# Optimization experiments

Measured on AMD Instinct MI355X. Metric: run time of the kernel, lower is better.

The kernel has to match this reference:

```python
import jax, jax.numpy as jnp
import numpy as np

W_IMPORTANCE = 0.1  # from __init__ default
EPS = 1e-12         # F.normalize eps


def _l2norm(x):
    n = jnp.sqrt(jnp.sum(x * x, axis=1, keepdims=True))
    return x / jnp.maximum(n, EPS)


def setup_inputs() -> dict:
    key = jax.random.key(0)
    k1, k2, k3 = jax.random.split(key, 3)
    return {
        "target_edge_feats": jax.random.normal(k1, (16384, 512), dtype=jnp.float32),
        "source_edge_feats": jax.random.normal(k2, (32768, 512), dtype=jnp.float32),
        "source_importance": jax.random.uniform(k3, (32768,), dtype=jnp.float32),
        "topk": 8,
        "chunk_size": 4096,
    }


def reference(target_edge_feats, source_edge_feats, source_importance, topk, chunk_size):
    E_t, Fdim = target_edge_feats.shape
    tn = _l2norm(target_edge_feats)            # [E_t, F]
    sn = _l2norm(source_edge_feats)            # [E_s, F]
    bias = W_IMPORTANCE * source_importance    # [E_s]

    n_chunks = E_t // chunk_size               # E_t chosen as exact multiple
    t_chunks = tn.reshape(n_chunks, chunk_size, Fdim)

    def per_chunk(t):
        # cosine similarity + importance bias, then top-k over sources
        score = jnp.einsum('cf,ef->ce', t, sn) + bias[None, :]  # [chunk, E_s]
        vals, idx = jax.lax.top_k(score, topk)
        return vals, idx

    vals, idx = jax.lax.map(per_chunk, t_chunks)  # [n_chunks, chunk, K]
    topk_score = vals.reshape(E_t, topk)
    topk_idx = idx.reshape(E_t, topk)
    topk_alpha = jax.nn.softmax(topk_score, axis=-1)
    return (topk_idx, topk_score, topk_alpha)
```

## Files before the change

### kernel.cpp

```cpp
#include <hip/hip_runtime.h>
#include <hip/hip_bf16.h>
#include <float.h>

#define KDIM 512
#define MBLK 64
#define NBLK 256
#define KBLK 16
#define NTH  256
#define APAD 68
#define BROW 284
#define TOPK 8
#define BIDX(c) ((c) + (((c) >> 5) << 2))

__device__ __forceinline__ float bf16_rne_f32(float v) {
  return __bfloat162float(__float2bfloat16(v));
}

__global__ void er_norms(const float* __restrict__ T, const float* __restrict__ S,
                         float* __restrict__ nt, float* __restrict__ ns,
                         int M, int N) {
  int gid = blockIdx.x * blockDim.x + threadIdx.x;
  int row = gid >> 2;
  int b   = gid & 3;
  if (row >= M + N) return;
  const float* base = (row < M) ? (T + (size_t)row * KDIM)
                                : (S + (size_t)(row - M) * KDIM);
  const float4* p4 = (const float4*)(base + b * 128);
  float r[8];
  {
    float4 f0 = p4[0], f1 = p4[1];
    r[0] = __fmul_rn(f0.x, f0.x); r[1] = __fmul_rn(f0.y, f0.y);
    r[2] = __fmul_rn(f0.z, f0.z); r[3] = __fmul_rn(f0.w, f0.w);
    r[4] = __fmul_rn(f1.x, f1.x); r[5] = __fmul_rn(f1.y, f1.y);
    r[6] = __fmul_rn(f1.z, f1.z); r[7] = __fmul_rn(f1.w, f1.w);
  }
  #pragma unroll
  for (int i = 2; i < 32; i += 2) {
    float4 f0 = p4[i], f1 = p4[i + 1];
    r[0] = __fadd_rn(r[0], __fmul_rn(f0.x, f0.x));
    r[1] = __fadd_rn(r[1], __fmul_rn(f0.y, f0.y));
    r[2] = __fadd_rn(r[2], __fmul_rn(f0.z, f0.z));
    r[3] = __fadd_rn(r[3], __fmul_rn(f0.w, f0.w));
    r[4] = __fadd_rn(r[4], __fmul_rn(f1.x, f1.x));
    r[5] = __fadd_rn(r[5], __fmul_rn(f1.y, f1.y));
    r[6] = __fadd_rn(r[6], __fmul_rn(f1.z, f1.z));
    r[7] = __fadd_rn(r[7], __fmul_rn(f1.w, f1.w));
  }
  float B = __fadd_rn(__fadd_rn(__fadd_rn(r[0], r[1]), __fadd_rn(r[2], r[3])),
                      __fadd_rn(__fadd_rn(r[4], r[5]), __fadd_rn(r[6], r[7])));
  float t = __fadd_rn(B, __shfl_xor(B, 1, 64));
  float s = __fadd_rn(t, __shfl_xor(t, 2, 64));
  if (b == 0) {
    float nr = __fsqrt_rn(s);
    if (row < M) nt[row] = nr; else ns[row - M] = nr;
  }
}

__global__ void er_prep(const float* __restrict__ X, const float* __restrict__ nrm,
                        float* __restrict__ XT, int R) {
  __shared__ float t[64][68];
  const int r0 = blockIdx.x * 64, c0 = blockIdx.y * 64;
  const int tx = threadIdx.x & 15, ty = threadIdx.x >> 4;
  #pragma unroll
  for (int q = 0; q < 4; ++q) {
    int r = r0 + ty + q * 16;
    float dn = fmaxf(nrm[r], 1e-12f);
    float4 v = *(const float4*)&X[(size_t)r * KDIM + c0 + tx * 4];
    t[ty + q*16][tx*4+0] = __fdiv_rn(v.x, dn);
    t[ty + q*16][tx*4+1] = __fdiv_rn(v.y, dn);
    t[ty + q*16][tx*4+2] = __fdiv_rn(v.z, dn);
    t[ty + q*16][tx*4+3] = __fdiv_rn(v.w, dn);
  }
  __syncthreads();
  #pragma unroll
  for (int q = 0; q < 4; ++q) {
    int c = c0 + ty + q * 16;
    float4 o;
    o.x = t[tx*4+0][ty + q*16];
    o.y = t[tx*4+1][ty + q*16];
    o.z = t[tx*4+2][ty + q*16];
    o.w = t[tx*4+3][ty + q*16];
    *(float4*)&XT[(size_t)c * R + r0 + tx * 4] = o;
  }
}

__global__ __launch_bounds__(NTH, 2)
void er_cand_fast(const float* __restrict__ ATN, const float* __restrict__ SNT,
                  const float* __restrict__ imp,
                  float* __restrict__ pval, int* __restrict__ pidx,
                  int M, int N, int nsplit, int mblocks) {
  __shared__ float b_lds[KBLK][NBLK];
  __shared__ float tval[MBLK][TOPK];
  __shared__ int   tidx[MBLK][TOPK];
  __shared__ float tthr[MBLK];

  const int tid    = threadIdx.x;
  const int mb     = blockIdx.x % mblocks;
  const int split  = blockIdx.x / mblocks;
  const int m_base = mb * MBLK;
  const int n_cols = N / nsplit;
  const int n_start = split * n_cols;
  const int ntiles  = n_cols / NBLK;
  const int lane = tid & 63;
  const int w = __builtin_amdgcn_readfirstlane(tid >> 6);

  if (tid < MBLK) {
    tthr[tid] = -FLT_MAX;
    #pragma unroll
    for (int j = 0; j < TOPK; ++j) { tval[tid][j] = -FLT_MAX; tidx[tid][j] = 0; }
  }
  __syncthreads();

  const float* aw = ATN + m_base + w * 16;

  #pragma unroll 1
  for (int t = 0; t < ntiles; ++t) {
    const int n_base = n_start + t * NBLK;
    float acc[16][4];
    #pragma unroll
    for (int i = 0; i < 16; ++i)
      #pragma unroll
      for (int j = 0; j < 4; ++j) acc[i][j] = 0.f;

    float4 br[4];
    #pragma unroll
    for (int ii = 0; ii < 4; ++ii)
      br[ii] = *(const float4*)&SNT[(size_t)(w + 4*ii) * N + n_base + lane * 4];

    #pragma unroll 1
    for (int kc = 0; kc < KDIM / KBLK; ++kc) {
      __syncthreads();
      #pragma unroll
      for (int ii = 0; ii < 4; ++ii)
        *(float4*)&b_lds[w + 4*ii][lane * 4] = br[ii];
      __syncthreads();
      if (kc + 1 < KDIM / KBLK) {
        #pragma unroll
        for (int ii = 0; ii < 4; ++ii)
          br[ii] = *(const float4*)&SNT[(size_t)((kc+1)*KBLK + w + 4*ii) * N
                                        + n_base + lane * 4];
      }
      #pragma unroll
      for (int k = 0; k < KBLK; ++k) {
        const float4* ap = (const float4*)(aw + (size_t)(kc * KBLK + k) * M);
        float4 a0 = ap[0], a1 = ap[1], a2 = ap[2], a3 = ap[3];
        float4 b  = *(const float4*)&b_lds[k][lane * 4];
        float av[16] = {a0.x,a0.y,a0.z,a0.w, a1.x,a1.y,a1.z,a1.w,
                        a2.x,a2.y,a2.z,a2.w, a3.x,a3.y,a3.z,a3.w};
        float bw4[4] = {b.x, b.y, b.z, b.w};
        #pragma unroll
        for (int i = 0; i < 16; ++i)
          #pragma unroll
          for (int j = 0; j < 4; ++j)
            acc[i][j] = fmaf(av[i], bw4[j], acc[i][j]);
      }
    }

    float4 impv = *(const float4*)&imp[n_base + lane * 4];
    float bv[4] = {__fmul_rn(0.1f, impv.x), __fmul_rn(0.1f, impv.y),
                   __fmul_rn(0.1f, impv.z), __fmul_rn(0.1f, impv.w)};
    int need = 0;
    #pragma unroll
    for (int i = 0; i < 16; ++i) {
      float thr = tthr[w * 16 + i];
      #pragma unroll
      for (int j = 0; j < 4; ++j) {
        float s = __fadd_rn(acc[i][j], bv[j]);
        need |= (s > thr) ? 1 : 0;
      }
    }
    unsigned long long mask = __ballot(need);
    while (mask) {
      int cur = __ffsll(mask) - 1;
      mask &= mask - 1;
      if (lane == cur) {
        #pragma unroll
        for (int i = 0; i < 16; ++i) {
          int r = w * 16 + i;
          #pragma unroll
          for (int j = 0; j < 4; ++j) {
            float s = __fadd_rn(acc[i][j], bv[j]);
            if (s > tthr[r]) {
              int p = TOPK - 1;
              while (p > 0 && tval[r][p-1] < s) {
                tval[r][p] = tval[r][p-1];
                tidx[r][p] = tidx[r][p-1];
                --p;
              }
              tval[r][p] = s;
              tidx[r][p] = n_base + lane * 4 + j;
              tthr[r] = tval[r][TOPK-1];
            }
          }
        }
      }
    }
  }

  __syncthreads();
  for (int r = tid; r < MBLK; r += NTH) {
    size_t off = ((size_t)split * M + m_base + r) * TOPK;
    #pragma unroll
    for (int j = 0; j < TOPK; ++j) { pval[off + j] = tval[r][j]; pidx[off + j] = tidx[r][j]; }
  }
}

__global__ __launch_bounds__(NTH, 2)
void er_cand_div(const float* __restrict__ A, const float* __restrict__ B,
                 const float* __restrict__ imp,
                 const float* __restrict__ nt, const float* __restrict__ ns,
                 float* __restrict__ pval, int* __restrict__ pidx,
                 int M, int N, int nsplit, int mblocks) {
  __shared__ float a_lds[KBLK][APAD];
  __shared__ float b_lds[KBLK][BROW];
  __shared__ float tval[MBLK][TOPK];
  __shared__ int   tidx[MBLK][TOPK];
  __shared__ float tthr[MBLK];

  const int tid    = threadIdx.x;
  const int mb     = blockIdx.x % mblocks;
  const int split  = blockIdx.x / mblocks;
  const int m_base = mb * MBLK;
  const int n_cols = N / nsplit;
  const int n_start = split * n_cols;
  const int ntiles  = n_cols / NBLK;
  const int tm = tid >> 5;
  const int tn = tid & 31;
  const int lane = tid & 63;

  if (tid < MBLK) {
    tthr[tid] = -FLT_MAX;
    #pragma unroll
    for (int j = 0; j < TOPK; ++j) { tval[tid][j] = -FLT_MAX; tidx[tid][j] = 0; }
  }
  __syncthreads();

  const int sarow = tid >> 2, saks = tid & 3;
  const int bread_off = BIDX(tn * 8);

  #pragma unroll 1
  for (int t = 0; t < ntiles; ++t) {
    const int n_base = n_start + t * NBLK;
    float acc[8][8];
    #pragma unroll
    for (int i = 0; i < 8; ++i)
      #pragma unroll
      for (int j = 0; j < 8; ++j) acc[i][j] = 0.f;

    float4 ar, br[4];
    ar = *(const float4*)&A[(size_t)(m_base + sarow) * KDIM + saks * 4];
    #pragma unroll
    for (int ii = 0; ii < 4; ++ii) {
      int u = tid + NTH * ii, row = u >> 2, ks = u & 3;
      br[ii] = *(const float4*)&B[(size_t)(n_base + row) * KDIM + ks * 4];
    }

    #pragma unroll 1
    for (int kc = 0; kc < KDIM / KBLK; ++kc) {
      __syncthreads();
      {
        float dn = fmaxf(nt[m_base + sarow], 1e-12f);
        a_lds[saks*4+0][sarow] = __fdiv_rn(ar.x, dn);
        a_lds[saks*4+1][sarow] = __fdiv_rn(ar.y, dn);
        a_lds[saks*4+2][sarow] = __fdiv_rn(ar.z, dn);
        a_lds[saks*4+3][sarow] = __fdiv_rn(ar.w, dn);
      }
      #pragma unroll
      for (int ii = 0; ii < 4; ++ii) {
        int u = tid + NTH * ii, row = u >> 2, ks = u & 3;
        float dn = fmaxf(ns[n_base + row], 1e-12f);
        int c = BIDX(row);
        b_lds[ks*4+0][c] = __fdiv_rn(br[ii].x, dn);
        b_lds[ks*4+1][c] = __fdiv_rn(br[ii].y, dn);
        b_lds[ks*4+2][c] = __fdiv_rn(br[ii].z, dn);
        b_lds[ks*4+3][c] = __fdiv_rn(br[ii].w, dn);
      }
      __syncthreads();
      if (kc + 1 < KDIM / KBLK) {
        int kb = (kc + 1) * KBLK;
        ar = *(const float4*)&A[(size_t)(m_base + sarow) * KDIM + kb + saks * 4];
        #pragma unroll
        for (int ii = 0; ii < 4; ++ii) {
          int u = tid + NTH * ii, row = u >> 2, ks = u & 3;
          br[ii] = *(const float4*)&B[(size_t)(n_base + row) * KDIM + kb + ks * 4];
        }
      }
      #pragma unroll 16
      for (int k = 0; k < KBLK; ++k) {
        const float4* ap = (const float4*)&a_lds[k][tm * 8];
        const float4* bp = (const float4*)&b_lds[k][bread_off];
        float4 a0 = ap[0], a1 = ap[1], b0 = bp[0], b1 = bp[1];
        float av[8] = {a0.x,a0.y,a0.z,a0.w,a1.x,a1.y,a1.z,a1.w};
        float bw[8] = {b0.x,b0.y,b0.z,b0.w,b1.x,b1.y,b1.z,b1.w};
        #pragma unroll
        for (int i = 0; i < 8; ++i)
          #pragma unroll
          for (int j = 0; j < 8; ++j)
            acc[i][j] = fmaf(av[i], bw[j], acc[i][j]);
      }
    }

    float bv[8];
    #pragma unroll
    for (int j = 0; j < 8; ++j) bv[j] = __fmul_rn(0.1f, imp[n_base + tn * 8 + j]);

    int need = 0;
    #pragma unroll
    for (int i = 0; i < 8; ++i) {
      float thr = tthr[tm * 8 + i];
      #pragma unroll
      for (int j = 0; j < 8; ++j) {
        float s = __fadd_rn(acc[i][j], bv[j]);
        need |= (s > thr) ? 1 : 0;
      }
    }
    unsigned long long mask = __ballot(need);
    while (mask) {
      int cur = __ffsll(mask) - 1;
      mask &= mask - 1;
      if (lane == cur) {
        #pragma unroll
        for (int i = 0; i < 8; ++i) {
          int r = tm * 8 + i;
          #pragma unroll
          for (int j = 0; j < 8; ++j) {
            float s = __fadd_rn(acc[i][j], bv[j]);
            if (s > tthr[r]) {
              int p = TOPK - 1;
              while (p > 0 && tval[r][p-1] < s) {
                tval[r][p] = tval[r][p-1];
                tidx[r][p] = tidx[r][p-1];
                --p;
              }
              tval[r][p] = s;
              tidx[r][p] = n_base + tn * 8 + j;
              tthr[r] = tval[r][TOPK-1];
            }
          }
        }
      }
    }
  }

  __syncthreads();
  for (int r = tid; r < MBLK; r += NTH) {
    size_t off = ((size_t)split * M + m_base + r) * TOPK;
    #pragma unroll
    for (int j = 0; j < TOPK; ++j) { pval[off + j] = tval[r][j]; pidx[off + j] = tidx[r][j]; }
  }
}

__global__ void er_merge(const float* __restrict__ pval, const int* __restrict__ pidx,
                         float* __restrict__ out, int M, int nsplit) {
  int m = blockIdx.x * blockDim.x + threadIdx.x;
  if (m >= M) return;
  int heads[4] = {0, 0, 0, 0};
  float v[TOPK]; int id[TOPK];
  for (int o = 0; o < TOPK; ++o) {
    float bvv = -FLT_MAX; int bi = 0x7fffffff; int bs = 0;
    for (int s = 0; s < nsplit; ++s) {
      if (heads[s] < TOPK) {
        size_t off = ((size_t)s * M + m) * TOPK + heads[s];
        float vv = pval[off]; int ii = pidx[off];
        if (vv > bvv || (vv == bvv && ii < bi)) { bvv = vv; bi = ii; bs = s; }
      }
    }
    v[o] = bvv; id[o] = bi; heads[bs]++;
  }
  float mx = v[0];
  float e[TOPK];
  #pragma unroll
  for (int j = 0; j < TOPK; ++j) e[j] = expf(__fadd_rn(v[j], -mx));
  float sum = __fadd_rn(
      __fadd_rn(__fadd_rn(e[0], e[1]), __fadd_rn(e[2], e[3])),
      __fadd_rn(__fadd_rn(e[4], e[5]), __fadd_rn(e[6], e[7])));
  const size_t SEC  = (size_t)M * TOPK;
  const size_t base = (size_t)m * TOPK;
  #pragma unroll
  for (int j = 0; j < TOPK; ++j) {
    out[base + j]         = bf16_rne_f32((float)id[j]);
    out[SEC + base + j]   = bf16_rne_f32(v[j]);
    out[2*SEC + base + j] = bf16_rne_f32(__fdiv_rn(e[j], sum));
  }
}

extern "C" void kernel_launch(void* const* d_in, const int* in_sizes, int n_in,
                              void* d_out, int out_size, void* d_ws, size_t ws_size,
                              hipStream_t stream) {
  const float* T   = (const float*)d_in[0];
  const float* S   = (const float*)d_in[1];
  const float* imp = (const float*)d_in[2];
  int M = in_sizes[0] / KDIM;
  int N = in_sizes[1] / KDIM;
  int mblocks = M / MBLK;

  char* ws = (char*)d_ws;
  float* nt = (float*)ws;
  float* ns = nt + M;
  size_t off_pval = (size_t)(M + N) * 4;
  size_t off_pidx = off_pval + (size_t)4 * M * TOPK * 4;
  size_t off_atn  = off_pidx + (size_t)4 * M * TOPK * 4;
  size_t off_snt  = off_atn + (size_t)M * KDIM * 4;
  size_t full_need = off_snt + (size_t)N * KDIM * 4;

  float* pval = (float*)(ws + off_pval);
  int*   pidx = (int*)(ws + off_pidx);
  float* out  = (float*)d_out;

  er_norms<<<(4 * (M + N) + 255) / 256, 256, 0, stream>>>(T, S, nt, ns, M, N);

  if (ws_size >= full_need) {
    float* ATN = (float*)(ws + off_atn);
    float* SNT = (float*)(ws + off_snt);
    er_prep<<<dim3(M / 64, KDIM / 64), 256, 0, stream>>>(T, nt, ATN, M);
    er_prep<<<dim3(N / 64, KDIM / 64), 256, 0, stream>>>(S, ns, SNT, N);
    er_cand_fast<<<mblocks * 4, NTH, 0, stream>>>(ATN, SNT, imp,
                                                  pval, pidx, M, N, 4, mblocks);
    er_merge<<<(M + 255) / 256, 256, 0, stream>>>(pval, pidx, out, M, 4);
  } else {
    int nsplit = 4;
    while (nsplit > 1) {
      size_t need = (size_t)(M + N) * 4 + (size_t)nsplit * M * TOPK * 8;
      if (need <= ws_size) break;
      nsplit >>= 1;
    }
    er_cand_div<<<mblocks * nsplit, NTH, 0, stream>>>(T, S, imp, nt, ns,
                                                      pval, pidx, M, N, nsplit, mblocks);
    er_merge<<<(M + 255) / 256, 256, 0, stream>>>(pval, pidx, out, M, nsplit);
  }
}
```

Measured before the change: 11.01 ms.

## Stage A tile in LDS and use 8x8 register blocking in candidate GEMM

The candidate-scoring kernel now stages the A (target) tile in shared memory alongside B, instead of each wave reading A directly from global memory every k step. Each thread computes an 8x8 register tile (8 rows by two groups of 4 columns) rather than 16x4, which improves arithmetic intensity per LDS load. The top-k insertion also gains index-based tie-breaking (lower index wins on equal scores) and uses >= in the filter, which may trigger the serial insertion path slightly more often.

```diff
diff --git a/kernel.cpp b/kernel.cpp
--- a/kernel.cpp
+++ b/kernel.cpp
@@ -85,10 +85,11 @@
 }
 
 __global__ __launch_bounds__(NTH, 2)
-void er_cand_fast(const float* __restrict__ ATN, const float* __restrict__ SNT,
-                  const float* __restrict__ imp,
-                  float* __restrict__ pval, int* __restrict__ pidx,
-                  int M, int N, int nsplit, int mblocks) {
+void er_cand_fast2(const float* __restrict__ ATN, const float* __restrict__ SNT,
+                   const float* __restrict__ imp,
+                   float* __restrict__ pval, int* __restrict__ pidx,
+                   int M, int N, int nsplit, int mblocks) {
+  __shared__ float a_lds[KBLK][APAD];
   __shared__ float b_lds[KBLK][NBLK];
   __shared__ float tval[MBLK][TOPK];
   __shared__ int   tidx[MBLK][TOPK];
@@ -101,72 +102,85 @@
   const int n_cols = N / nsplit;
   const int n_start = split * n_cols;
   const int ntiles  = n_cols / NBLK;
+  const int tm = tid >> 5;
+  const int tn = tid & 31;
   const int lane = tid & 63;
-  const int w = __builtin_amdgcn_readfirstlane(tid >> 6);
 
   if (tid < MBLK) {
     tthr[tid] = -FLT_MAX;
     #pragma unroll
-    for (int j = 0; j < TOPK; ++j) { tval[tid][j] = -FLT_MAX; tidx[tid][j] = 0; }
+    for (int j = 0; j < TOPK; ++j) { tval[tid][j] = -FLT_MAX; tidx[tid][j] = 0x7fffffff; }
   }
   __syncthreads();
 
-  const float* aw = ATN + m_base + w * 16;
+  const int arow = tid >> 4, acol = (tid & 15) * 4;
 
   #pragma unroll 1
   for (int t = 0; t < ntiles; ++t) {
     const int n_base = n_start + t * NBLK;
-    float acc[16][4];
-    #pragma unroll
-    for (int i = 0; i < 16; ++i)
-      #pragma unroll
-      for (int j = 0; j < 4; ++j) acc[i][j] = 0.f;
-
-    float4 br[4];
-    #pragma unroll
-    for (int ii = 0; ii < 4; ++ii)
-      br[ii] = *(const float4*)&SNT[(size_t)(w + 4*ii) * N + n_base + lane * 4];
+    float acc[8][8];
+    #pragma unroll
+    for (int i = 0; i < 8; ++i)
+      #pragma unroll
+      for (int j = 0; j < 8; ++j) acc[i][j] = 0.f;
+
+    float4 ar, br[4];
+    ar = *(const float4*)&ATN[(size_t)arow * M + m_base + acol];
+    #pragma unroll
+    for (int ii = 0; ii < 4; ++ii) {
+      int u = tid + NTH * ii, brow = u >> 6, bcol = (u & 63) * 4;
+      br[ii] = *(const float4*)&SNT[(size_t)brow * N + n_base + bcol];
+    }
 
     #pragma unroll 1
     for (int kc = 0; kc < KDIM / KBLK; ++kc) {
       __syncthreads();
-      #pragma unroll
-      for (int ii = 0; ii < 4; ++ii)
-        *(float4*)&b_lds[w + 4*ii][lane * 4] = br[ii];
+      *(float4*)&a_lds[arow][acol] = ar;
+      #pragma unroll
+      for (int ii = 0; ii < 4; ++ii) {
+        int u = tid + NTH * ii, brow = u >> 6, bcol = (u & 63) * 4;
+        *(float4*)&b_lds[brow][bcol] = br[ii];
+      }
       __syncthreads();
       if (kc + 1 < KDIM / KBLK) {
-        #pragma unroll
-        for (int ii = 0; ii < 4; ++ii)
-          br[ii] = *(const float4*)&SNT[(size_t)((kc+1)*KBLK + w + 4*ii) * N
-                                        + n_base + lane * 4];
+        int kb = (kc + 1) * KBLK;
+        ar = *(const float4*)&ATN[(size_t)(kb + arow) * M + m_base + acol];
+        #pragma unroll
+        for (int ii = 0; ii < 4; ++ii) {
+          int u = tid + NTH * ii, brow = u >> 6, bcol = (u & 63) * 4;
+          br[ii] = *(const float4*)&SNT[(size_t)(kb + brow) * N + n_base + bcol];
+        }
       }
       #pragma unroll
       for (int k = 0; k < KBLK; ++k) {
-        const float4* ap = (const float4*)(aw + (size_t)(kc * KBLK + k) * M);
-        float4 a0 = ap[0], a1 = ap[1], a2 = ap[2], a3 = ap[3];
-        float4 b  = *(const float4*)&b_lds[k][lane * 4];
-        float av[16] = {a0.x,a0.y,a0.z,a0.w, a1.x,a1.y,a1.z,a1.w,
-                        a2.x,a2.y,a2.z,a2.w, a3.x,a3.y,a3.z,a3.w};
-        float bw4[4] = {b.x, b.y, b.z, b.w};
-        #pragma unroll
-        for (int i = 0; i < 16; ++i)
+        const float4* ap = (const float4*)&a_lds[k][tm * 8];
+        float4 a0 = ap[0], a1 = ap[1];
+        float4 b0 = *(const float4*)&b_lds[k][tn * 4];
+        float4 b1 = *(const float4*)&b_lds[k][128 + tn * 4];
+        float av[8] = {a0.x,a0.y,a0.z,a0.w,a1.x,a1.y,a1.z,a1.w};
+        float bw[8] = {b0.x,b0.y,b0.z,b0.w,b1.x,b1.y,b1.z,b1.w};
+        #pragma unroll
+        for (int i = 0; i < 8; ++i)
           #pragma unroll
-          for (int j = 0; j < 4; ++j)
-            acc[i][j] = fmaf(av[i], bw4[j], acc[i][j]);
-      }
-    }
-
-    float4 impv = *(const float4*)&imp[n_base + lane * 4];
-    float bv[4] = {__fmul_rn(0.1f, impv.x), __fmul_rn(0.1f, impv.y),
-                   __fmul_rn(0.1f, impv.z), __fmul_rn(0.1f, impv.w)};
+          for (int j = 0; j < 8; ++j)
+            acc[i][j] = fmaf(av[i], bw[j], acc[i][j]);
+      }
+    }
+
+    float4 i0 = *(const float4*)&imp[n_base + tn * 4];
+    float4 i1 = *(const float4*)&imp[n_base + 128 + tn * 4];
+    float bv[8] = {__fmul_rn(0.1f, i0.x), __fmul_rn(0.1f, i0.y),
+                   __fmul_rn(0.1f, i0.z), __fmul_rn(0.1f, i0.w),
+                   __fmul_rn(0.1f, i1.x), __fmul_rn(0.1f, i1.y),
+                   __fmul_rn(0.1f, i1.z), __fmul_rn(0.1f, i1.w)};
     int need = 0;
     #pragma unroll
-    for (int i = 0; i < 16; ++i) {
-      float thr = tthr[w * 16 + i];
-      #pragma unroll
-      for (int j = 0; j < 4; ++j) {
+    for (int i = 0; i < 8; ++i) {
+      float thr = tthr[tm * 8 + i];
+      #pragma unroll
+      for (int j = 0; j < 8; ++j) {
         float s = __fadd_rn(acc[i][j], bv[j]);
-        need |= (s > thr) ? 1 : 0;
+        need |= (s >= thr) ? 1 : 0;
       }
     }
     unsigned long long mask = __ballot(need);
@@ -175,20 +189,23 @@
       mask &= mask - 1;
       if (lane == cur) {
         #pragma unroll
-        for (int i = 0; i < 16; ++i) {
-          int r = w * 16 + i;
+        for (int i = 0; i < 8; ++i) {
+          int r = tm * 8 + i;
           #pragma unroll
-          for (int j = 0; j < 4; ++j) {
+          for (int j = 0; j < 8; ++j) {
             float s = __fadd_rn(acc[i][j], bv[j]);
-            if (s > tthr[r]) {
+            int  n = n_base + ((j < 4) ? (tn * 4 + j) : (128 + tn * 4 + j - 4));
+            float v8 = tval[r][TOPK-1]; int i8 = tidx[r][TOPK-1];
+            if (s > v8 || (s == v8 && n < i8)) {
               int p = TOPK - 1;
-              while (p > 0 && tval[r][p-1] < s) {
+              while (p > 0 && (tval[r][p-1] < s ||
+                               (tval[r][p-1] == s && tidx[r][p-1] > n))) {
                 tval[r][p] = tval[r][p-1];
                 tidx[r][p] = tidx[r][p-1];
                 --p;
               }
               tval[r][p] = s;
-              tidx[r][p] = n_base + lane * 4 + j;
+              tidx[r][p] = n;
               tthr[r] = tval[r][TOPK-1];
             }
           }
@@ -414,8 +431,8 @@
     float* SNT = (float*)(ws + off_snt);
     er_prep<<<dim3(M / 64, KDIM / 64), 256, 0, stream>>>(T, nt, ATN, M);
     er_prep<<<dim3(N / 64, KDIM / 64), 256, 0, stream>>>(S, ns, SNT, N);
-    er_cand_fast<<<mblocks * 4, NTH, 0, stream>>>(ATN, SNT, imp,
-                                                  pval, pidx, M, N, 4, mblocks);
+    er_cand_fast2<<<mblocks * 4, NTH, 0, stream>>>(ATN, SNT, imp,
+                                                   pval, pidx, M, N, 4, mblocks);
     er_merge<<<(M + 255) / 256, 256, 0, stream>>>(pval, pidx, out, M, 4);
   } else {
     int nsplit = 4;
```

Result: slower. 12.61 ms (+14.6%).
